# Kernel optimization log

Measured on AMD Instinct MI355X. Metric: run time of the kernel, lower is better.

Reference implementation:

```python
import jax, jax.numpy as jnp
import numpy as np

B, T = 1024, 8192


def setup_inputs() -> dict:
    key = jax.random.key(0)
    k1, k2 = jax.random.split(key)
    # phi/psi are [B, T, 2] probability-bound robustness traces in [0, 1]
    phi = jax.random.uniform(k1, (B, T, 2), dtype=jnp.float32)
    psi = jax.random.uniform(k2, (B, T, 2), dtype=jnp.float32)
    return {"phi": phi, "psi": psi}


def reference(phi, psi):
    """Until operator, interval [0, inf), exact (scale<=0) min/max.

    Original O(T^2) double loop computes, for each t:
        out[t] = max_{tau in [t, T-1]} min( min(phi[t..tau-1]), psi[tau] )
    with the empty segment (tau == t) contributing min(ones, psi[t]).
    Because min distributes over max, this satisfies the exact O(T)
    backward recurrence:
        r[t] = max( min(1, psi[t]), min(phi[t], r[t+1]) ),  r[T] = -inf
    which we evaluate with a reversed lax.scan over the time axis.
    """
    phi_t = jnp.swapaxes(phi, 0, 1)  # [T, B, 2]
    psi_t = jnp.swapaxes(psi, 0, 1)  # [T, B, 2]

    def step(carry, xs):
        p, q = xs
        v = jnp.minimum(jnp.asarray(1.0, p.dtype), q)  # tau == t term (min with ones)
        r = jnp.maximum(v, jnp.minimum(p, carry))
        return r, r

    init = jnp.full(phi_t.shape[1:], -jnp.inf, dtype=phi.dtype)  # [B, 2]
    _, out = jax.lax.scan(step, init, (phi_t, psi_t), reverse=True)
    return jnp.swapaxes(out, 0, 1)  # [B, T, 2]
```

## Files before the change

kernel.cpp:

```cpp
#include <hip/hip_runtime.h>


#define T_LEN 8192
#define NSEG  8
#define BLOCK (NSEG * 64)

__device__ __forceinline__ float rfl(float x) {
    return __int_as_float(__builtin_amdgcn_readfirstlane(__float_as_int(x)));
}

__device__ __forceinline__ void wave_lds_fence() {
    __asm__ volatile("" ::: "memory");
    __builtin_amdgcn_wave_barrier();
    __asm__ volatile("" ::: "memory");
}

__global__ __launch_bounds__(BLOCK, 4) void until_kernel(
    const float* __restrict__ phi, const float* __restrict__ psi,
    float* __restrict__ out)
{
    const int  row  = blockIdx.x;
    const int  tid  = threadIdx.x;
    const int  w    = tid >> 6;
    const int  lane = tid & 63;
    const float NEG = -__builtin_huge_valf();
    const float POS =  __builtin_huge_valf();

    const size_t segf4 = (size_t)row * (T_LEN / 2) + (size_t)w * 512;
    const float4* __restrict__ phi4 = (const float4*)phi + segf4;
    const float4* __restrict__ psi4 = (const float4*)psi + segf4;
    float4* __restrict__ out4 = (float4*)out + segf4;

    __shared__ alignas(16) float lds[NSEG * 2048];
    __shared__ float4 ssum[NSEG];
    float* wl = lds + w * 2048;

    float4 P[8], Q[8];
#pragma unroll
    for (int k = 0; k < 8; ++k) {
        P[k] = phi4[k * 64 + lane];
        Q[k] = psi4[k * 64 + lane];
    }

#pragma unroll
    for (int k = 0; k < 8; ++k) {
        const int r  = k >> 2;
        const int kl = k & 3;
        float* base = wl + r * 1024 + kl * 64 + lane;
        float v0x = fminf(1.f, Q[k].x), v0y = fminf(1.f, Q[k].y);
        float v1x = fminf(1.f, Q[k].z), v1y = fminf(1.f, Q[k].w);
        base[0]   = fmaxf(v0x, fminf(P[k].x, v1x));
        base[256] = fmaxf(v0y, fminf(P[k].y, v1y));
        base[512] = fminf(P[k].x, P[k].z);
        base[768] = fminf(P[k].y, P[k].w);
    }
    wave_lds_fence();

    float4 GAx[2], GAy[2], GBx[2], GBy[2];
    float  Sax[2], Say[2], Sbx[2], Sby[2];
#pragma unroll
    for (int r = 0; r < 2; ++r) {
        const float* rb = wl + r * 1024;
        GAx[r] = *(const float4*)(rb + 0 * 256 + lane * 4);
        GAy[r] = *(const float4*)(rb + 1 * 256 + lane * 4);
        GBx[r] = *(const float4*)(rb + 2 * 256 + lane * 4);
        GBy[r] = *(const float4*)(rb + 3 * 256 + lane * 4);

        float hax = GAx[r].w, hay = GAy[r].w, hbx = GBx[r].w, hby = GBy[r].w;
        hax = fmaxf(GAx[r].z, fminf(GBx[r].z, hax));
        hay = fmaxf(GAy[r].z, fminf(GBy[r].z, hay));
        hbx = fminf(GBx[r].z, hbx);
        hby = fminf(GBy[r].z, hby);
        hax = fmaxf(GAx[r].y, fminf(GBx[r].y, hax));
        hay = fmaxf(GAy[r].y, fminf(GBy[r].y, hay));
        hbx = fminf(GBx[r].y, hbx);
        hby = fminf(GBy[r].y, hby);
        hax = fmaxf(GAx[r].x, fminf(GBx[r].x, hax));
        hay = fmaxf(GAy[r].x, fminf(GBy[r].x, hay));
        hbx = fminf(GBx[r].x, hbx);
        hby = fminf(GBy[r].x, hby);

#pragma unroll
        for (int off = 1; off < 64; off <<= 1) {
            float gax = __shfl_down(hax, off), gay = __shfl_down(hay, off);
            float gbx = __shfl_down(hbx, off), gby = __shfl_down(hby, off);
            bool  val = (lane + off) < 64;
            gax = val ? gax : NEG;  gay = val ? gay : NEG;
            gbx = val ? gbx : POS;  gby = val ? gby : POS;
            hax = fmaxf(hax, fminf(hbx, gax));
            hay = fmaxf(hay, fminf(hby, gay));
            hbx = fminf(hbx, gbx);
            hby = fminf(hby, gby);
        }
        Sax[r] = hax; Say[r] = hay; Sbx[r] = hbx; Sby[r] = hby;
    }

    float R0ax = rfl(Sax[0]), R0ay = rfl(Say[0]);
    float R0bx = rfl(Sbx[0]), R0by = rfl(Sby[0]);
    float R1ax = rfl(Sax[1]), R1ay = rfl(Say[1]);
    float R1bx = rfl(Sbx[1]), R1by = rfl(Sby[1]);
    if (lane == 0) {
        float wax = fmaxf(R0ax, fminf(R0bx, R1ax));
        float way = fmaxf(R0ay, fminf(R0by, R1ay));
        float wbx = fminf(R0bx, R1bx);
        float wby = fminf(R0by, R1by);
        ssum[w] = make_float4(wax, way, wbx, wby);
    }
    __syncthreads();
    float rcx = NEG, rcy = NEG;
    for (int j = NSEG - 1; j > w; --j) {
        float4 s = ssum[j];
        rcx = fmaxf(s.x, fminf(s.z, rcx));
        rcy = fmaxf(s.y, fminf(s.w, rcy));
    }

    float rinx[2], riny[2];
    rinx[1] = rcx;
    riny[1] = rcy;
    rinx[0] = fmaxf(R1ax, fminf(R1bx, rcx));
    riny[0] = fmaxf(R1ay, fminf(R1by, rcy));

#pragma unroll
    for (int r = 0; r < 2; ++r) {
        float yx = fmaxf(Sax[r], fminf(Sbx[r], rinx[r]));
        float yy = fmaxf(Say[r], fminf(Sby[r], riny[r]));
        float cx = __shfl_down(yx, 1), cy = __shfl_down(yy, 1);
        if (lane == 63) { cx = rinx[r]; cy = riny[r]; }
        float4 CX, CY;
        CX.w = cx;
        CY.w = cy;
        CX.z = fmaxf(GAx[r].w, fminf(GBx[r].w, CX.w));
        CY.z = fmaxf(GAy[r].w, fminf(GBy[r].w, CY.w));
        CX.y = fmaxf(GAx[r].z, fminf(GBx[r].z, CX.z));
        CY.y = fmaxf(GAy[r].z, fminf(GBy[r].z, CY.z));
        CX.x = fmaxf(GAx[r].y, fminf(GBx[r].y, CX.y));
        CY.x = fmaxf(GAy[r].y, fminf(GBy[r].y, CY.y));
        *(float4*)(wl +       r * 256 + lane * 4) = CX;
        *(float4*)(wl + 512 + r * 256 + lane * 4) = CY;
    }
    wave_lds_fence();

#pragma unroll
    for (int k = 0; k < 8; ++k) {
        const int e = k * 64 + lane;
        float4 P2 = phi4[e];
        float4 Q2 = psi4[e];
        float cx = wl[e];
        float cy = wl[512 + e];
        float r1x = fmaxf(fminf(1.f, Q2.z), fminf(P2.z, cx));
        float r1y = fmaxf(fminf(1.f, Q2.w), fminf(P2.w, cy));
        float r0x = fmaxf(fminf(1.f, Q2.x), fminf(P2.x, r1x));
        float r0y = fmaxf(fminf(1.f, Q2.y), fminf(P2.y, r1y));
        out4[e] = make_float4(r0x, r0y, r1x, r1y);
    }
}

extern "C" void kernel_launch(void* const* d_in, const int* in_sizes, int n_in,
                              void* d_out, int out_size, void* d_ws, size_t ws_size,
                              hipStream_t stream) {
    const float* phi = (const float*)d_in[0];
    const float* psi = (const float*)d_in[1];
    float* out = (float*)d_out;
    const int Bn = in_sizes[0] / (T_LEN * 2);
    until_kernel<<<Bn, BLOCK, 0, stream>>>(phi, psi, out);
}
```

Baseline: 180.3 us.

## Split until scan into separate segment-sum and apply kernels

Replaces the single per-row kernel, which used a block-wide barrier to combine segment summaries, with two kernels. The first computes per-wave segment compositions into a workspace. The second reads them, folds the suffix, recomputes the local scan and writes the output. This removes the intra-block sync and cuts the LDS footprint per block to raise occupancy, at the cost of reading the inputs again from global memory and redoing the local scan work.

```diff
diff --git a/kernel.cpp b/kernel.cpp
--- a/kernel.cpp
+++ b/kernel.cpp
@@ -1,9 +1,12 @@
 #include <hip/hip_runtime.h>
 
 
-#define T_LEN 8192
-#define NSEG  8
-#define BLOCK (NSEG * 64)
+#define T_LEN  8192
+#define ROW_F4 (T_LEN / 2)
+#define SEG_F4 512
+#define NSEG   8
+#define BLK    256
+#define WPB    (BLK / 64)
 
 __device__ __forceinline__ float rfl(float x) {
     return __int_as_float(__builtin_amdgcn_readfirstlane(__float_as_int(x)));
@@ -15,25 +18,121 @@
     __asm__ volatile("" ::: "memory");
 }
 
-__global__ __launch_bounds__(BLOCK, 4) void until_kernel(
-    const float* __restrict__ phi, const float* __restrict__ psi,
-    float* __restrict__ out)
+__device__ __forceinline__ void build_G(const float4& P, const float4& Q,
+                                        float* base) {
+    float v0x = fminf(1.f, Q.x), v0y = fminf(1.f, Q.y);
+    float v1x = fminf(1.f, Q.z), v1y = fminf(1.f, Q.w);
+    base[0]   = fmaxf(v0x, fminf(P.x, v1x));
+    base[256] = fmaxf(v0y, fminf(P.y, v1y));
+    base[512] = fminf(P.x, P.z);
+    base[768] = fminf(P.y, P.w);
+}
+
+__device__ __forceinline__ void compose_scan(
+    const float4& gax, const float4& gay, const float4& gbx, const float4& gby,
+    int lane, float& Sax, float& Say, float& Sbx, float& Sby)
 {
-    const int  row  = blockIdx.x;
-    const int  tid  = threadIdx.x;
-    const int  w    = tid >> 6;
-    const int  lane = tid & 63;
     const float NEG = -__builtin_huge_valf();
     const float POS =  __builtin_huge_valf();
-
-    const size_t segf4 = (size_t)row * (T_LEN / 2) + (size_t)w * 512;
+    float hax = gax.w, hay = gay.w, hbx = gbx.w, hby = gby.w;
+    hax = fmaxf(gax.z, fminf(gbx.z, hax));
+    hay = fmaxf(gay.z, fminf(gby.z, hay));
+    hbx = fminf(gbx.z, hbx);
+    hby = fminf(gby.z, hby);
+    hax = fmaxf(gax.y, fminf(gbx.y, hax));
+    hay = fmaxf(gay.y, fminf(gby.y, hay));
+    hbx = fminf(gbx.y, hbx);
+    hby = fminf(gby.y, hby);
+    hax = fmaxf(gax.x, fminf(gbx.x, hax));
+    hay = fmaxf(gay.x, fminf(gby.x, hay));
+    hbx = fminf(gbx.x, hbx);
+    hby = fminf(gby.x, hby);
+#pragma unroll
+    for (int off = 1; off < 64; off <<= 1) {
+        float qax = __shfl_down(hax, off), qay = __shfl_down(hay, off);
+        float qbx = __shfl_down(hbx, off), qby = __shfl_down(hby, off);
+        bool  val = (lane + off) < 64;
+        qax = val ? qax : NEG;  qay = val ? qay : NEG;
+        qbx = val ? qbx : POS;  qby = val ? qby : POS;
+        hax = fmaxf(hax, fminf(hbx, qax));
+        hay = fmaxf(hay, fminf(hby, qay));
+        hbx = fminf(hbx, qbx);
+        hby = fminf(hby, qby);
+    }
+    Sax = hax; Say = hay; Sbx = hbx; Sby = hby;
+}
+
+__global__ __launch_bounds__(BLK, 4) void until_sum(
+    const float* __restrict__ phi, const float* __restrict__ psi,
+    float4* __restrict__ ws4)
+{
+    const int wid  = blockIdx.x * WPB + (threadIdx.x >> 6);
+    const int row  = wid >> 3;
+    const int w    = wid & 7;
+    const int lane = threadIdx.x & 63;
+
+    const size_t segf4 = (size_t)row * ROW_F4 + (size_t)w * SEG_F4;
+    const float4* __restrict__ phi4 = (const float4*)phi + segf4;
+    const float4* __restrict__ psi4 = (const float4*)psi + segf4;
+
+    __shared__ alignas(16) float lds[WPB * 1024];
+    float* wl = lds + (threadIdx.x >> 6) * 1024;
+
+    float4 P[8], Q[8];
+#pragma unroll
+    for (int k = 0; k < 8; ++k) {
+        P[k] = phi4[k * 64 + lane];
+        Q[k] = psi4[k * 64 + lane];
+    }
+
+    float Sax[2], Say[2], Sbx[2], Sby[2];
+#pragma unroll
+    for (int r = 0; r < 2; ++r) {
+#pragma unroll
+        for (int kl = 0; kl < 4; ++kl)
+            build_G(P[r * 4 + kl], Q[r * 4 + kl], wl + kl * 64 + lane);
+        wave_lds_fence();
+        float4 gax = *(const float4*)(wl + 0 * 256 + lane * 4);
+        float4 gay = *(const float4*)(wl + 1 * 256 + lane * 4);
+        float4 gbx = *(const float4*)(wl + 2 * 256 + lane * 4);
+        float4 gby = *(const float4*)(wl + 3 * 256 + lane * 4);
+        wave_lds_fence();
+        compose_scan(gax, gay, gbx, gby, lane, Sax[r], Say[r], Sbx[r], Sby[r]);
+    }
+    if (lane == 0) {
+        float wax = fmaxf(Sax[0], fminf(Sbx[0], Sax[1]));
+        float way = fmaxf(Say[0], fminf(Sby[0], Say[1]));
+        float wbx = fminf(Sbx[0], Sbx[1]);
+        float wby = fminf(Sby[0], Sby[1]);
+        ws4[wid] = make_float4(wax, way, wbx, wby);
+    }
+}
+
+__global__ __launch_bounds__(BLK, 4) void until_apply(
+    const float* __restrict__ phi, const float* __restrict__ psi,
+    const float4* __restrict__ ws4, float* __restrict__ out)
+{
+    const int wid  = blockIdx.x * WPB + (threadIdx.x >> 6);
+    const int row  = wid >> 3;
+    const int w    = wid & 7;
+    const int lane = threadIdx.x & 63;
+    const float NEG = -__builtin_huge_valf();
+
+    const size_t segf4 = (size_t)row * ROW_F4 + (size_t)w * SEG_F4;
     const float4* __restrict__ phi4 = (const float4*)phi + segf4;
     const float4* __restrict__ psi4 = (const float4*)psi + segf4;
     float4* __restrict__ out4 = (float4*)out + segf4;
 
-    __shared__ alignas(16) float lds[NSEG * 2048];
-    __shared__ float4 ssum[NSEG];
-    float* wl = lds + w * 2048;
+    __shared__ alignas(16) float lds[WPB * 1024];
+    float* wl = lds + (threadIdx.x >> 6) * 1024;
+
+    const float4* __restrict__ sums = ws4 + (size_t)row * NSEG;
+    float rcx = NEG, rcy = NEG;
+    for (int j = NSEG - 1; j > w; --j) {
+        float4 s = sums[j];
+        rcx = fmaxf(s.x, fminf(s.z, rcx));
+        rcy = fmaxf(s.y, fminf(s.w, rcy));
+    }
 
     float4 P[8], Q[8];
 #pragma unroll
@@ -42,78 +141,25 @@
         Q[k] = psi4[k * 64 + lane];
     }
 
-#pragma unroll
-    for (int k = 0; k < 8; ++k) {
-        const int r  = k >> 2;
-        const int kl = k & 3;
-        float* base = wl + r * 1024 + kl * 64 + lane;
-        float v0x = fminf(1.f, Q[k].x), v0y = fminf(1.f, Q[k].y);
-        float v1x = fminf(1.f, Q[k].z), v1y = fminf(1.f, Q[k].w);
-        base[0]   = fmaxf(v0x, fminf(P[k].x, v1x));
-        base[256] = fmaxf(v0y, fminf(P[k].y, v1y));
-        base[512] = fminf(P[k].x, P[k].z);
-        base[768] = fminf(P[k].y, P[k].w);
-    }
-    wave_lds_fence();
-
     float4 GAx[2], GAy[2], GBx[2], GBy[2];
     float  Sax[2], Say[2], Sbx[2], Sby[2];
 #pragma unroll
     for (int r = 0; r < 2; ++r) {
-        const float* rb = wl + r * 1024;
-        GAx[r] = *(const float4*)(rb + 0 * 256 + lane * 4);
-        GAy[r] = *(const float4*)(rb + 1 * 256 + lane * 4);
-        GBx[r] = *(const float4*)(rb + 2 * 256 + lane * 4);
-        GBy[r] = *(const float4*)(rb + 3 * 256 + lane * 4);
-
-        float hax = GAx[r].w, hay = GAy[r].w, hbx = GBx[r].w, hby = GBy[r].w;
-        hax = fmaxf(GAx[r].z, fminf(GBx[r].z, hax));
-        hay = fmaxf(GAy[r].z, fminf(GBy[r].z, hay));
-        hbx = fminf(GBx[r].z, hbx);
-        hby = fminf(GBy[r].z, hby);
-        hax = fmaxf(GAx[r].y, fminf(GBx[r].y, hax));
-        hay = fmaxf(GAy[r].y, fminf(GBy[r].y, hay));
-        hbx = fminf(GBx[r].y, hbx);
-        hby = fminf(GBy[r].y, hby);
-        hax = fmaxf(GAx[r].x, fminf(GBx[r].x, hax));
-        hay = fmaxf(GAy[r].x, fminf(GBy[r].x, hay));
-        hbx = fminf(GBx[r].x, hbx);
-        hby = fminf(GBy[r].x, hby);
-
-#pragma unroll
-        for (int off = 1; off < 64; off <<= 1) {
-            float gax = __shfl_down(hax, off), gay = __shfl_down(hay, off);
-            float gbx = __shfl_down(hbx, off), gby = __shfl_down(hby, off);
-            bool  val = (lane + off) < 64;
-            gax = val ? gax : NEG;  gay = val ? gay : NEG;
-            gbx = val ? gbx : POS;  gby = val ? gby : POS;
-            hax = fmaxf(hax, fminf(hbx, gax));
-            hay = fmaxf(hay, fminf(hby, gay));
-            hbx = fminf(hbx, gbx);
-            hby = fminf(hby, gby);
-        }
-        Sax[r] = hax; Say[r] = hay; Sbx[r] = hbx; Sby[r] = hby;
-    }
-
-    float R0ax = rfl(Sax[0]), R0ay = rfl(Say[0]);
-    float R0bx = rfl(Sbx[0]), R0by = rfl(Sby[0]);
+#pragma unroll
+        for (int kl = 0; kl < 4; ++kl)
+            build_G(P[r * 4 + kl], Q[r * 4 + kl], wl + kl * 64 + lane);
+        wave_lds_fence();
+        GAx[r] = *(const float4*)(wl + 0 * 256 + lane * 4);
+        GAy[r] = *(const float4*)(wl + 1 * 256 + lane * 4);
+        GBx[r] = *(const float4*)(wl + 2 * 256 + lane * 4);
+        GBy[r] = *(const float4*)(wl + 3 * 256 + lane * 4);
+        wave_lds_fence();
+        compose_scan(GAx[r], GAy[r], GBx[r], GBy[r], lane,
+                     Sax[r], Say[r], Sbx[r], Sby[r]);
+    }
+
     float R1ax = rfl(Sax[1]), R1ay = rfl(Say[1]);
     float R1bx = rfl(Sbx[1]), R1by = rfl(Sby[1]);
-    if (lane == 0) {
-        float wax = fmaxf(R0ax, fminf(R0bx, R1ax));
-        float way = fmaxf(R0ay, fminf(R0by, R1ay));
-        float wbx = fminf(R0bx, R1bx);
-        float wby = fminf(R0by, R1by);
-        ssum[w] = make_float4(wax, way, wbx, wby);
-    }
-    __syncthreads();
-    float rcx = NEG, rcy = NEG;
-    for (int j = NSEG - 1; j > w; --j) {
-        float4 s = ssum[j];
-        rcx = fmaxf(s.x, fminf(s.z, rcx));
-        rcy = fmaxf(s.y, fminf(s.w, rcy));
-    }
-
     float rinx[2], riny[2];
     rinx[1] = rcx;
     riny[1] = rcy;
@@ -161,6 +207,10 @@
     const float* phi = (const float*)d_in[0];
     const float* psi = (const float*)d_in[1];
     float* out = (float*)d_out;
+    float4* ws4 = (float4*)d_ws;
     const int Bn = in_sizes[0] / (T_LEN * 2);
-    until_kernel<<<Bn, BLOCK, 0, stream>>>(phi, psi, out);
-}
+    const int nwaves = Bn * NSEG;
+    const int grid = nwaves / WPB;
+    until_sum<<<grid, BLK, 0, stream>>>(phi, psi, ws4);
+    until_apply<<<grid, BLK, 0, stream>>>(phi, psi, ws4, out);
+}
```

Result: slower. 208.9 us (+15.9%).
